# Optimization experiments

Hardware: AMD Instinct MI355X
Metric: run time of the kernel (lower is better)

## Reference

```python
import jax, jax.numpy as jnp
import numpy as np

N = 50000  # nodes == edges (source multiplies [N,H] node tensor by [E] edge attention)
HW = 8


def _adaptive_pool_2x2_from9(h):
    # PyTorch AdaptiveAvgPool2d((2,2)) on 9x9: bins [0:5) and [4:9) per dim (overlap at 4)
    def binpair(t, ax):
        s0 = jnp.take(t, jnp.arange(0, 5), axis=ax).mean(axis=ax)
        s1 = jnp.take(t, jnp.arange(4, 9), axis=ax).mean(axis=ax)
        return jnp.stack([s0, s1], axis=ax)
    return binpair(binpair(h, 3), 2)  # [N,64,2,2]


def _fe_net(x, c1w, c1b, c2w, c2b, fw, fb):
    h = x[:, None, :, :]  # [N,1,8,8]
    h = jax.lax.conv_general_dilated(h, c1w, (1, 1), ((1, 1), (1, 1)),
                                     dimension_numbers=('NCHW', 'OIHW', 'NCHW')) + c1b[None, :, None, None]
    h = jax.nn.relu(h)  # [N,32,8,8]
    h = jax.lax.conv_general_dilated(h, c2w, (1, 1), ((1, 1), (1, 1)),
                                     dimension_numbers=('NCHW', 'OIHW', 'NCHW')) + c2b[None, :, None, None]
    h = jax.nn.relu(h)  # [N,64,9,9]
    h = _adaptive_pool_2x2_from9(h).reshape(h.shape[0], -1)  # [N,256]
    return h @ fw + fb  # [N,32]


def _gcn(x, src, dst, W, b, n):
    h = x @ W
    idx = jnp.arange(n)
    s = jnp.concatenate([src, idx])
    d = jnp.concatenate([dst, idx])
    deg = jax.ops.segment_sum(jnp.ones(s.shape[0], h.dtype), d, num_segments=n)
    dis = jnp.where(deg > 0, jax.lax.rsqrt(jnp.maximum(deg, 1e-12)), 0.0)
    norm = dis[s] * dis[d]
    out = jax.ops.segment_sum(h[s] * norm[:, None], d, num_segments=n)
    return out + b


def _attention1(aux, src, dst, n):
    frame = aux[:, 2]
    fd = jnp.abs(frame[src] - frame[dst])
    outdeg = jax.ops.segment_sum(jnp.ones(src.shape[0], aux.dtype), src, num_segments=n)
    return jnp.where(fd == 1.0, 1.0 / jnp.maximum(outdeg[src], 1.0), 0.0)


def _attention2(aux, src, dst):
    ang, rad, frame = aux[:, 0], aux[:, 1], aux[:, 2]
    fd = jnp.abs(frame[src] - frame[dst])
    dx = rad[dst] * jnp.cos(ang[dst]) - rad[src] * jnp.cos(ang[src])
    dy = rad[dst] * jnp.sin(ang[dst]) - rad[src] * jnp.sin(ang[src])
    fd_safe = jnp.where(fd == 2.0, fd, 1.0)
    vel = jnp.sqrt(dx * dx + dy * dy + 1e-12) / fd_safe
    return jnp.where(fd == 2.0, jnp.exp(-vel / 8.5), 0.0)


def setup_inputs() -> dict:
    key = jax.random.key(0)
    ks = jax.random.split(key, 20)
    x = jax.random.normal(ks[0], (N, HW, HW), jnp.float32)
    angle = jax.random.uniform(ks[1], (N,), jnp.float32, 0.0, 2.0 * np.pi)
    radius = jax.random.uniform(ks[2], (N,), jnp.float32, 1.0, 100.0)
    frame = jax.random.randint(ks[3], (N,), 0, 10).astype(jnp.float32)
    aux_features = jnp.stack([angle, radius, frame], axis=1)
    edge_index = jax.random.randint(ks[4], (2, N), 0, N)
    s = 0.05
    p = lambda k, sh: jax.random.normal(k, sh, jnp.float32) * s
    return {
        'x': x, 'aux_features': aux_features, 'edge_index': edge_index,
        'conv1_w': p(ks[5], (32, 1, 3, 3)), 'conv1_b': jnp.zeros((32,), jnp.float32),
        'conv2_w': p(ks[6], (64, 32, 2, 2)), 'conv2_b': jnp.zeros((64,), jnp.float32),
        'fe_fc_w': p(ks[7], (256, 32)), 'fe_fc_b': jnp.zeros((32,), jnp.float32),
        'gcn1_w': p(ks[8], (32, 64)), 'gcn1_b': jnp.zeros((64,), jnp.float32),
        'gcn2_w': p(ks[9], (64, 64)), 'gcn2_b': jnp.zeros((64,), jnp.float32),
        'fc_w': p(ks[10], (64, 32)), 'fc_b': jnp.zeros((32,), jnp.float32),
        'out_w': p(ks[11], (32, 1)), 'out_b': jnp.zeros((1,), jnp.float32),
    }


def reference(x, aux_features, edge_index, conv1_w, conv1_b, conv2_w, conv2_b,
              fe_fc_w, fe_fc_b, gcn1_w, gcn1_b, gcn2_w, gcn2_b, fc_w, fc_b,
              out_w, out_b):
    n = x.shape[0]
    src, dst = edge_index[0], edge_index[1]
    sig = _fe_net(x, conv1_w, conv1_b, conv2_w, conv2_b, fe_fc_w, fe_fc_b)  # [N,32]
    att1 = _attention1(aux_features, src, dst, n)  # [E] == [N]
    x1 = jax.nn.relu(_gcn(sig, src, dst, gcn1_w, gcn1_b, n) * att1[:, None])
    att2 = _attention2(aux_features, src, dst)
    x2 = jax.nn.relu(_gcn(x1, src, dst, gcn2_w, gcn2_b, n) * att2[:, None])
    h = jax.nn.relu(x2 @ fc_w + fc_b)
    out = jax.nn.sigmoid(h @ out_w + out_b)  # [N,1]
    return out
```

## Files before the change

kernel.cpp:

```cpp
#include <hip/hip_runtime.h>
#include <math.h>

typedef float f32x4 __attribute__((ext_vector_type(4)));
typedef __bf16 bf16x8 __attribute__((ext_vector_type(8)));
typedef unsigned short ushort8 __attribute__((ext_vector_type(8)));
typedef unsigned short ushort4v __attribute__((ext_vector_type(4)));

static __device__ __forceinline__ unsigned short f2bf(float f) {
    unsigned int u = __builtin_bit_cast(unsigned int, f);
    unsigned int lsb = (u >> 16) & 1u;
    u += 0x7fffu + lsb;
    return (unsigned short)(u >> 16);
}

__global__ __launch_bounds__(256, 3) void fe_kernel(
    const float* __restrict__ x,
    const float* __restrict__ w1, const float* __restrict__ b1,
    const float* __restrict__ w2, const float* __restrict__ b2,
    unsigned short* __restrict__ poolbf, int n)
{
    __shared__ float w1t[10][32];
    __shared__ unsigned short hT[4][100][40];
    __shared__ float xs[4][104];

    const int t = threadIdx.x, lane = t & 63, wave = t >> 6;
    const int cl = lane & 15, kg = lane >> 4;

    if (t < 288) w1t[t >> 5][t & 31] = w1[(t & 31) * 9 + (t >> 5)];
    if (t >= 288 && t < 320) w1t[9][t - 288] = b1[t - 288];

    bf16x8 bfr[4][4];
    #pragma unroll
    for (int ct = 0; ct < 4; ++ct)
        #pragma unroll
        for (int tap = 0; tap < 4; ++tap) {
            const float* gp = w2 + (size_t)(ct * 16 + cl) * 128 + kg * 32 + tap;
            ushort8 u;
            #pragma unroll
            for (int e = 0; e < 8; ++e) u[e] = f2bf(gp[e * 4]);
            bfr[ct][tap] = __builtin_bit_cast(bf16x8, u);
        }
    float b2r[4];
    #pragma unroll
    for (int ct = 0; ct < 4; ++ct) b2r[ct] = b2[ct * 16 + cl];

    {
        ushort8 z8 = {0,0,0,0,0,0,0,0};
        for (int r = lane; r < 100; r += 64) {
            const int pi = r / 10, pj = r - 10 * (r / 10);
            if (pi == 0 || pi == 9 || pj == 0 || pj == 9) {
                *reinterpret_cast<ushort8*>(&hT[wave][r][0])  = z8;
                *reinterpret_cast<ushort8*>(&hT[wave][r][8])  = z8;
                *reinterpret_cast<ushort8*>(&hT[wave][r][16]) = z8;
                *reinterpret_cast<ushort8*>(&hT[wave][r][24]) = z8;
                xs[wave][r] = 0.0f;
            }
        }
    }
    __syncthreads();

    const int i = lane >> 3, j = lane & 7;
    const int rr = (i + 1) * 10 + (j + 1);
    const int gw = blockIdx.x * 4 + wave;
    const int nw = gridDim.x * 4;

    for (int node = gw; node < n; node += nw) {
        xs[wave][rr] = x[(size_t)node * 64 + lane];
        asm volatile("s_waitcnt lgkmcnt(0)" ::: "memory");

        float xv[9];
        #pragma unroll
        for (int ki = 0; ki < 3; ++ki)
            #pragma unroll
            for (int kj = 0; kj < 3; ++kj)
                xv[ki * 3 + kj] = xs[wave][(i + ki) * 10 + (j + kj)];

        #pragma unroll
        for (int cp = 0; cp < 4; ++cp) {
            ushort8 hv;
            #pragma unroll
            for (int half = 0; half < 2; ++half) {
                const int cg = cp * 2 + half;
                f32x4 s = *reinterpret_cast<const f32x4*>(&w1t[9][cg * 4]);
                #pragma unroll
                for (int q = 0; q < 9; ++q) {
                    const f32x4 wq = *reinterpret_cast<const f32x4*>(&w1t[q][cg * 4]);
                    s += xv[q] * wq;
                }
                #pragma unroll
                for (int c = 0; c < 4; ++c)
                    hv[half * 4 + c] = f2bf(fmaxf(s[c], 0.0f));
            }
            *reinterpret_cast<ushort8*>(&hT[wave][rr][cp * 8]) = hv;
        }
        asm volatile("s_waitcnt lgkmcnt(0)" ::: "memory");

        float pb[4][4];
        #pragma unroll
        for (int ct = 0; ct < 4; ++ct)
            #pragma unroll
            for (int b = 0; b < 4; ++b) pb[ct][b] = 0.0f;

        #pragma unroll
        for (int mt = 0; mt < 6; ++mt) {
            const int p = mt * 16 + cl;
            const int ia = p / 9, ja = p - ia * 9;
            const int rb = (p < 81) ? (ia * 10 + ja) : 0;

            f32x4 acc[4];
            #pragma unroll
            for (int ct = 0; ct < 4; ++ct)
                acc[ct] = (f32x4){b2r[ct], b2r[ct], b2r[ct], b2r[ct]};

            #pragma unroll
            for (int tap = 0; tap < 4; ++tap) {
                const bf16x8 afr = *reinterpret_cast<const bf16x8*>(
                    &hT[wave][rb + (tap >> 1) * 10 + (tap & 1)][kg * 8]);
                #pragma unroll
                for (int ct = 0; ct < 4; ++ct)
                    acc[ct] = __builtin_amdgcn_mfma_f32_16x16x32_bf16(
                        afr, bfr[ct][tap], acc[ct], 0, 0, 0);
            }

            #pragma unroll
            for (int rg = 0; rg < 4; ++rg) {
                if (mt * 16 + rg >= 81) continue;
                const int pd = mt * 16 + (kg << 2) + rg;
                const int id = pd / 9, jd = pd - id * 9;
                const bool val = pd < 81;
                const float wa = (val && id <= 4 && jd <= 4) ? 1.0f : 0.0f;
                const float wb = (val && id <= 4 && jd >= 4) ? 1.0f : 0.0f;
                const float wc = (val && id >= 4 && jd <= 4) ? 1.0f : 0.0f;
                const float wd = (val && id >= 4 && jd >= 4) ? 1.0f : 0.0f;
                #pragma unroll
                for (int ct = 0; ct < 4; ++ct) {
                    const float v = fmaxf(acc[ct][rg], 0.0f);
                    pb[ct][0] = fmaf(v, wa, pb[ct][0]);
                    pb[ct][1] = fmaf(v, wb, pb[ct][1]);
                    pb[ct][2] = fmaf(v, wc, pb[ct][2]);
                    pb[ct][3] = fmaf(v, wd, pb[ct][3]);
                }
            }
        }

        #pragma unroll
        for (int ct = 0; ct < 4; ++ct)
            #pragma unroll
            for (int b = 0; b < 4; ++b) {
                pb[ct][b] += __shfl_xor(pb[ct][b], 16);
                pb[ct][b] += __shfl_xor(pb[ct][b], 32);
            }
        ushort4v pv;
        #pragma unroll
        for (int b = 0; b < 4; ++b) {
            const float q = (kg == 0) ? pb[0][b] : (kg == 1) ? pb[1][b]
                          : (kg == 2) ? pb[2][b] : pb[3][b];
            pv[b] = f2bf(q);
        }
        *reinterpret_cast<ushort4v*>(poolbf + (size_t)node * 256 + lane * 4) = pv;
    }
}

__global__ void pre_k(const float* __restrict__ fw, const float* __restrict__ fb,
                      const float* __restrict__ g1w, const float* __restrict__ g2w,
                      unsigned short* __restrict__ W1t, float* __restrict__ v1,
                      unsigned short* __restrict__ W2t)
{
    const int b = blockIdx.x, t = threadIdx.x;
    if (b < 64) {
        float s = 0.0f;
        for (int jj = 0; jj < 32; ++jj) s += fw[t * 32 + jj] * g1w[jj * 64 + b];
        W1t[b * 256 + t] = f2bf(0.04f * s);
    } else {
        const int idx = (b - 64) * 256 + t;
        const int nc = idx >> 6, k = idx & 63;
        W2t[nc * 64 + k] = f2bf(g2w[k * 64 + nc]);
        if (b == 64 && t < 64) {
            float s = 0.0f;
            for (int jj = 0; jj < 32; ++jj) s += fb[jj] * g1w[jj * 64 + t];
            v1[t] = s;
        }
    }
}

template<int NKS, bool HASV>
__global__ __launch_bounds__(256) void mm_k(
    const unsigned short* __restrict__ A, const unsigned short* __restrict__ Bt,
    const float* __restrict__ v1, float* __restrict__ h, int n)
{
    const int lane = threadIdx.x & 63;
    const int cl = lane & 15, kg = lane >> 4;
    const int gw = blockIdx.x * 4 + (threadIdx.x >> 6);
    const int nw = gridDim.x * 4;
    const int K = NKS * 32;
    const int ntiles = (n + 15) >> 4;

    float vv[4];
    #pragma unroll
    for (int nt = 0; nt < 4; ++nt) vv[nt] = HASV ? v1[nt * 16 + cl] : 0.0f;

    for (int mt = gw; mt < ntiles; mt += nw) {
        const int r = min(mt * 16 + cl, n - 1);
        const unsigned short* ar = A + (size_t)r * K + kg * 8;
        f32x4 acc[4];
        #pragma unroll
        for (int nt = 0; nt < 4; ++nt)
            acc[nt] = (f32x4){vv[nt], vv[nt], vv[nt], vv[nt]};
        #pragma unroll
        for (int ks = 0; ks < NKS; ++ks) {
            const bf16x8 afr = *reinterpret_cast<const bf16x8*>(ar + ks * 32);
            #pragma unroll
            for (int nt = 0; nt < 4; ++nt) {
                const bf16x8 bfr = *reinterpret_cast<const bf16x8*>(
                    Bt + (size_t)(nt * 16 + cl) * K + ks * 32 + kg * 8);
                acc[nt] = __builtin_amdgcn_mfma_f32_16x16x32_bf16(afr, bfr, acc[nt], 0, 0, 0);
            }
        }
        #pragma unroll
        for (int nt = 0; nt < 4; ++nt)
            #pragma unroll
            for (int rg = 0; rg < 4; ++rg) {
                const int row = mt * 16 + (kg << 2) + rg;
                if (row < n) h[(size_t)row * 64 + nt * 16 + cl] = acc[nt][rg];
            }
    }
}

__global__ void zero_k(float* __restrict__ p, int n)
{
    int idx = blockIdx.x * blockDim.x + threadIdx.x;
    if (idx < n) p[idx] = 0.0f;
}

__global__ void count_k(const int* __restrict__ ei, float* __restrict__ outdeg,
                        float* __restrict__ indeg, int m)
{
    int e = blockIdx.x * blockDim.x + threadIdx.x;
    if (e >= m) return;
    atomicAdd(&outdeg[ei[e]], 1.0f);
    atomicAdd(&indeg[ei[m + e]], 1.0f);
}

__global__ void prep_k(const float* __restrict__ indeg, float* __restrict__ dis, int n)
{
    int idx = blockIdx.x * blockDim.x + threadIdx.x;
    if (idx < n) dis[idx] = rsqrtf(indeg[idx] + 1.0f);
}

__global__ void att_k(const float* __restrict__ aux, const int* __restrict__ ei,
                      const float* __restrict__ outdeg,
                      float* __restrict__ att1, float* __restrict__ att2, int m)
{
    int e = blockIdx.x * blockDim.x + threadIdx.x;
    if (e >= m) return;
    const int s = ei[e], d = ei[m + e];
    const float fs = aux[(size_t)s * 3 + 2], fdd = aux[(size_t)d * 3 + 2];
    const float fd = fabsf(fs - fdd);
    att1[e] = (fd == 1.0f) ? (1.0f / fmaxf(outdeg[s], 1.0f)) : 0.0f;
    const float angs = aux[(size_t)s * 3 + 0], rads = aux[(size_t)s * 3 + 1];
    const float angd = aux[(size_t)d * 3 + 0], radd = aux[(size_t)d * 3 + 1];
    const float dx = radd * cosf(angd) - rads * cosf(angs);
    const float dy = radd * sinf(angd) - rads * sinf(angs);
    const float vel = sqrtf(dx * dx + dy * dy + 1e-12f) * 0.5f;
    att2[e] = (fd == 2.0f) ? expf(-vel / 8.5f) : 0.0f;
}

__global__ void accinit_k(const float* __restrict__ h, const float* __restrict__ dis,
                          const float* __restrict__ b, float* __restrict__ acc, int n)
{
    size_t idx = (size_t)blockIdx.x * blockDim.x + threadIdx.x;
    if (idx >= (size_t)n * 64) return;
    const int node = (int)(idx >> 6), k = (int)(idx & 63);
    const float di = dis[node];
    acc[idx] = b[k] + di * di * h[idx];
}

__global__ void scatter_k(const float* __restrict__ h, const int* __restrict__ ei,
                          const float* __restrict__ dis, float* __restrict__ acc, int m)
{
    size_t idx = (size_t)blockIdx.x * blockDim.x + threadIdx.x;
    if (idx >= (size_t)m * 64) return;
    const int e = (int)(idx >> 6), k = (int)(idx & 63);
    const int s = ei[e], d = ei[m + e];
    const float w = dis[s] * dis[d];
    atomicAdd(&acc[(size_t)d * 64 + k], w * h[(size_t)s * 64 + k]);
}

__global__ void fin_k(float* __restrict__ acc, const float* __restrict__ att,
                      unsigned short* __restrict__ xout, int n)
{
    size_t idx = (size_t)blockIdx.x * blockDim.x + threadIdx.x;
    if (idx >= (size_t)n * 64) return;
    const int node = (int)(idx >> 6);
    const float v = fmaxf(acc[idx] * att[node], 0.0f);
    if (xout) xout[idx] = f2bf(v);
    else      acc[idx] = v;
}

__global__ void head_k(const float* __restrict__ x2, const float* __restrict__ fcw,
                       const float* __restrict__ fcb, const float* __restrict__ outw,
                       const float* __restrict__ outb, float* __restrict__ out, int n)
{
    size_t idx = (size_t)blockIdx.x * blockDim.x + threadIdx.x;
    const int node = (int)(idx >> 5), o = (int)(idx & 31);
    if (node >= n) return;
    const float* xr = x2 + (size_t)node * 64;
    float s = fcb[o];
    #pragma unroll
    for (int k = 0; k < 64; ++k) s = fmaf(xr[k], fcw[k * 32 + o], s);
    s = fmaxf(s, 0.0f);
    float p = s * outw[o];
    #pragma unroll
    for (int mk = 16; mk >= 1; mk >>= 1) p += __shfl_xor(p, mk);
    if (o == 0) out[node] = 1.0f / (1.0f + expf(-(p + outb[0])));
}

extern "C" void kernel_launch(void* const* d_in, const int* in_sizes, int n_in,
                              void* d_out, int out_size, void* d_ws, size_t ws_size,
                              hipStream_t stream)
{
    const float* x    = (const float*)d_in[0];
    const float* aux  = (const float*)d_in[1];
    const int*   ei   = (const int*)  d_in[2];
    const float* c1w  = (const float*)d_in[3];
    const float* c1b  = (const float*)d_in[4];
    const float* c2w  = (const float*)d_in[5];
    const float* c2b  = (const float*)d_in[6];
    const float* few  = (const float*)d_in[7];
    const float* feb  = (const float*)d_in[8];
    const float* g1w  = (const float*)d_in[9];
    const float* g1b  = (const float*)d_in[10];
    const float* g2w  = (const float*)d_in[11];
    const float* g2b  = (const float*)d_in[12];
    const float* fcw  = (const float*)d_in[13];
    const float* fcb  = (const float*)d_in[14];
    const float* outw = (const float*)d_in[15];
    const float* outb = (const float*)d_in[16];
    float* out = (float*)d_out;

    const int n = in_sizes[0] / 64;
    const int m = in_sizes[2] / 2;

    float* ws = (float*)d_ws;
    unsigned short* poolbf = (unsigned short*)ws;
    float* acc  = ws;
    unsigned short* x1bf = (unsigned short*)(ws + (size_t)n * 64);
    float* h    = ws + (size_t)n * 128;
    unsigned short* W1t = (unsigned short*)(ws + (size_t)n * 192);
    float* v1   = ws + (size_t)n * 192 + 8192;
    unsigned short* W2t = (unsigned short*)(v1 + 64);
    float* outdeg = v1 + 64 + 2048;
    float* indeg  = outdeg + n;
    float* dis    = indeg + n;
    float* att1   = dis + n;
    float* att2   = att1 + m;

    const dim3 b256(256);
    const int gE   = (m + 255) / 256;
    const int gNn  = (n + 255) / 256;
    const int gNM  = (int)(((size_t)n * 64 + 255) / 256);
    const int gEM  = (int)(((size_t)m * 64 + 255) / 256);
    const int gNH  = (int)(((size_t)n * 32 + 255) / 256);
    const int gMM  = (((n + 15) / 16) + 3) / 4;

    pre_k<<<80, b256, 0, stream>>>(few, feb, g1w, g2w, W1t, v1, W2t);
    fe_kernel<<<768, b256, 0, stream>>>(x, c1w, c1b, c2w, c2b, poolbf, n);

    zero_k<<<(2 * n + 255) / 256, b256, 0, stream>>>(outdeg, 2 * n);
    count_k<<<gE, b256, 0, stream>>>(ei, outdeg, indeg, m);
    prep_k<<<gNn, b256, 0, stream>>>(indeg, dis, n);
    att_k<<<gE, b256, 0, stream>>>(aux, ei, outdeg, att1, att2, m);

    mm_k<8, true><<<gMM, b256, 0, stream>>>(poolbf, W1t, v1, h, n);
    accinit_k<<<gNM, b256, 0, stream>>>(h, dis, g1b, acc, n);
    scatter_k<<<gEM, b256, 0, stream>>>(h, ei, dis, acc, m);
    fin_k<<<gNM, b256, 0, stream>>>(acc, att1, x1bf, n);

    mm_k<2, false><<<gMM, b256, 0, stream>>>(x1bf, W2t, nullptr, h, n);
    accinit_k<<<gNM, b256, 0, stream>>>(h, dis, g2b, acc, n);
    scatter_k<<<gEM, b256, 0, stream>>>(h, ei, dis, acc, m);
    fin_k<<<gNM, b256, 0, stream>>>(acc, att2, nullptr, n);

    head_k<<<gNH, b256, 0, stream>>>(acc, fcw, fcb, outw, outb, out, n);
}
```

Baseline: 287.0 us.

## Move conv1 to MFMA via im2col, prefetch inputs, and streamline pooling reduction

The first 3x3 convolution now builds a per-wave im2col tile through lane shuffles and runs it as bf16 MFMA instead of scalar FMAs over LDS. The next node's input row is prefetched in a register, and the pooling bin masks and conv2 row bases are computed once and held in registers. The cross-lane pooling reduction now uses a transposed exchange that halves the shuffle count. It also switches to the hardware bf16 convert and zeroes all of LDS without a block barrier. This aims to cut VALU work in fe_kernel, at the cost of conv1 inputs being rounded to bf16 and more register pressure.

```diff
diff --git a/kernel.cpp b/kernel.cpp
--- a/kernel.cpp
+++ b/kernel.cpp
@@ -2,15 +2,13 @@
 #include <math.h>
 
 typedef float f32x4 __attribute__((ext_vector_type(4)));
+typedef float f32x2 __attribute__((ext_vector_type(2)));
 typedef __bf16 bf16x8 __attribute__((ext_vector_type(8)));
 typedef unsigned short ushort8 __attribute__((ext_vector_type(8)));
 typedef unsigned short ushort4v __attribute__((ext_vector_type(4)));
 
-static __device__ __forceinline__ unsigned short f2bf(float f) {
-    unsigned int u = __builtin_bit_cast(unsigned int, f);
-    unsigned int lsb = (u >> 16) & 1u;
-    u += 0x7fffu + lsb;
-    return (unsigned short)(u >> 16);
+static __device__ __forceinline__ unsigned short bfbits(float f) {
+    return __builtin_bit_cast(unsigned short, (__bf16)f);
 }
 
 __global__ __launch_bounds__(256, 3) void fe_kernel(
@@ -19,145 +17,187 @@
     const float* __restrict__ w2, const float* __restrict__ b2,
     unsigned short* __restrict__ poolbf, int n)
 {
-    __shared__ float w1t[10][32];
     __shared__ unsigned short hT[4][100][40];
-    __shared__ float xs[4][104];
+    __shared__ unsigned short xim[4][64][40];
 
     const int t = threadIdx.x, lane = t & 63, wave = t >> 6;
     const int cl = lane & 15, kg = lane >> 4;
-
-    if (t < 288) w1t[t >> 5][t & 31] = w1[(t & 31) * 9 + (t >> 5)];
-    if (t >= 288 && t < 320) w1t[9][t - 288] = b1[t - 288];
-
-    bf16x8 bfr[4][4];
-    #pragma unroll
-    for (int ct = 0; ct < 4; ++ct)
+    const int i = lane >> 3, j = lane & 7;
+
+    for (int e = lane; e < 100 * 40; e += 64) (&hT[wave][0][0])[e] = 0;
+    for (int e = lane; e < 64 * 40; e += 64) (&xim[wave][0][0])[e] = 0;
+
+    bf16x8 w1f[2]; float b1r[2];
+    #pragma unroll
+    for (int ct = 0; ct < 2; ++ct) {
+        ushort8 u;
+        #pragma unroll
+        for (int e = 0; e < 8; ++e) {
+            const int tap = kg * 8 + e;
+            u[e] = (tap < 9) ? bfbits(w1[(ct * 16 + cl) * 9 + tap]) : (unsigned short)0;
+        }
+        w1f[ct] = __builtin_bit_cast(bf16x8, u);
+        b1r[ct] = b1[ct * 16 + cl];
+    }
+
+    bf16x8 bfr[4][4]; float b2r[4];
+    #pragma unroll
+    for (int ct = 0; ct < 4; ++ct) {
         #pragma unroll
         for (int tap = 0; tap < 4; ++tap) {
-            const float* gp = w2 + (size_t)(ct * 16 + cl) * 128 + kg * 32 + tap;
             ushort8 u;
             #pragma unroll
-            for (int e = 0; e < 8; ++e) u[e] = f2bf(gp[e * 4]);
+            for (int e = 0; e < 8; ++e) {
+                const int pos = kg * 8 + e;
+                const int ci = ((pos & 1) << 4) | (pos >> 1);
+                u[e] = bfbits(w2[(size_t)(ct * 16 + cl) * 128 + ci * 4 + tap]);
+            }
             bfr[ct][tap] = __builtin_bit_cast(bf16x8, u);
         }
-    float b2r[4];
-    #pragma unroll
-    for (int ct = 0; ct < 4; ++ct) b2r[ct] = b2[ct * 16 + cl];
-
+        b2r[ct] = b2[ct * 16 + cl];
+    }
+
+    ushort8 vmask; unsigned short m8;
     {
-        ushort8 z8 = {0,0,0,0,0,0,0,0};
-        for (int r = lane; r < 100; r += 64) {
-            const int pi = r / 10, pj = r - 10 * (r / 10);
-            if (pi == 0 || pi == 9 || pj == 0 || pj == 9) {
-                *reinterpret_cast<ushort8*>(&hT[wave][r][0])  = z8;
-                *reinterpret_cast<ushort8*>(&hT[wave][r][8])  = z8;
-                *reinterpret_cast<ushort8*>(&hT[wave][r][16]) = z8;
-                *reinterpret_cast<ushort8*>(&hT[wave][r][24]) = z8;
-                xs[wave][r] = 0.0f;
-            }
-        }
-    }
-    __syncthreads();
-
-    const int i = lane >> 3, j = lane & 7;
-    const int rr = (i + 1) * 10 + (j + 1);
+        #pragma unroll
+        for (int q = 0; q < 9; ++q) {
+            const int ki = q / 3, kj = q - 3 * (q / 3);
+            const int ri = i + ki - 1, cj = j + kj - 1;
+            const unsigned short ok = (ri >= 0 && ri < 8 && cj >= 0 && cj < 8) ? 0xFFFFu : 0;
+            if (q < 8) vmask[q] = ok; else m8 = ok;
+        }
+    }
+
+    unsigned int pm[3] = {0u, 0u, 0u};
+    #pragma unroll
+    for (int mt = 0; mt < 6; ++mt)
+        #pragma unroll
+        for (int rg = 0; rg < 4; ++rg) {
+            const int slot = mt * 4 + rg;
+            const int pd = mt * 16 + kg * 4 + rg;
+            unsigned int bits = 0;
+            if (pd < 81) {
+                const int id = pd / 9, jd = pd - 9 * (pd / 9);
+                if (id <= 4 && jd <= 4) bits |= 1u;
+                if (id <= 4 && jd >= 4) bits |= 2u;
+                if (id >= 4 && jd <= 4) bits |= 4u;
+                if (id >= 4 && jd >= 4) bits |= 8u;
+            }
+            pm[slot >> 3] |= bits << ((slot & 7) * 4);
+        }
+
+    int rbase[6];
+    #pragma unroll
+    for (int mt = 0; mt < 6; ++mt) {
+        const int p = mt * 16 + cl;
+        const int ia = p / 9, ja = p - 9 * ia;
+        rbase[mt] = (p < 81) ? (ia * 10 + ja) : 0;
+    }
+
     const int gw = blockIdx.x * 4 + wave;
     const int nw = gridDim.x * 4;
 
+    float v = (gw < n) ? x[(size_t)gw * 64 + lane] : 0.0f;
+
     for (int node = gw; node < n; node += nw) {
-        xs[wave][rr] = x[(size_t)node * 64 + lane];
+        const int nn = node + nw;
+        const float vnext = x[(size_t)(nn < n ? nn : node) * 64 + lane];
+
+        float tv[9];
+        tv[0] = __shfl(v, lane - 9); tv[1] = __shfl(v, lane - 8); tv[2] = __shfl(v, lane - 7);
+        tv[3] = __shfl(v, lane - 1); tv[4] = v;                   tv[5] = __shfl(v, lane + 1);
+        tv[6] = __shfl(v, lane + 7); tv[7] = __shfl(v, lane + 8); tv[8] = __shfl(v, lane + 9);
+        ushort8 pk;
+        #pragma unroll
+        for (int q = 0; q < 8; ++q) pk[q] = bfbits(tv[q]);
+        pk &= vmask;
+        *reinterpret_cast<ushort8*>(&xim[wave][lane][0]) = pk;
+        xim[wave][lane][8] = bfbits(tv[8]) & m8;
+
         asm volatile("s_waitcnt lgkmcnt(0)" ::: "memory");
 
-        float xv[9];
-        #pragma unroll
-        for (int ki = 0; ki < 3; ++ki)
-            #pragma unroll
-            for (int kj = 0; kj < 3; ++kj)
-                xv[ki * 3 + kj] = xs[wave][(i + ki) * 10 + (j + kj)];
-
-        #pragma unroll
-        for (int cp = 0; cp < 4; ++cp) {
-            ushort8 hv;
-            #pragma unroll
-            for (int half = 0; half < 2; ++half) {
-                const int cg = cp * 2 + half;
-                f32x4 s = *reinterpret_cast<const f32x4*>(&w1t[9][cg * 4]);
-                #pragma unroll
-                for (int q = 0; q < 9; ++q) {
-                    const f32x4 wq = *reinterpret_cast<const f32x4*>(&w1t[q][cg * 4]);
-                    s += xv[q] * wq;
-                }
-                #pragma unroll
-                for (int c = 0; c < 4; ++c)
-                    hv[half * 4 + c] = f2bf(fmaxf(s[c], 0.0f));
-            }
-            *reinterpret_cast<ushort8*>(&hT[wave][rr][cp * 8]) = hv;
+        #pragma unroll
+        for (int mt = 0; mt < 4; ++mt) {
+            const bf16x8 afr = *reinterpret_cast<const bf16x8*>(&xim[wave][mt * 16 + cl][kg * 8]);
+            f32x4 a0 = {b1r[0], b1r[0], b1r[0], b1r[0]};
+            f32x4 a1 = {b1r[1], b1r[1], b1r[1], b1r[1]};
+            a0 = __builtin_amdgcn_mfma_f32_16x16x32_bf16(afr, w1f[0], a0, 0, 0, 0);
+            a1 = __builtin_amdgcn_mfma_f32_16x16x32_bf16(afr, w1f[1], a1, 0, 0, 0);
+            #pragma unroll
+            for (int rg = 0; rg < 4; ++rg) {
+                const int pdx = mt * 16 + kg * 4 + rg;
+                const int row = ((pdx >> 3) + 1) * 10 + (pdx & 7) + 1;
+                const unsigned int packed =
+                    (unsigned int)bfbits(fmaxf(a0[rg], 0.0f)) |
+                    ((unsigned int)bfbits(fmaxf(a1[rg], 0.0f)) << 16);
+                *reinterpret_cast<unsigned int*>(&hT[wave][row][cl * 2]) = packed;
+            }
         }
         asm volatile("s_waitcnt lgkmcnt(0)" ::: "memory");
 
-        float pb[4][4];
-        #pragma unroll
-        for (int ct = 0; ct < 4; ++ct)
-            #pragma unroll
-            for (int b = 0; b < 4; ++b) pb[ct][b] = 0.0f;
+        f32x2 pb01[4], pb23[4];
+        #pragma unroll
+        for (int ct = 0; ct < 4; ++ct) { pb01[ct] = (f32x2){0.f, 0.f}; pb23[ct] = (f32x2){0.f, 0.f}; }
 
         #pragma unroll
         for (int mt = 0; mt < 6; ++mt) {
-            const int p = mt * 16 + cl;
-            const int ia = p / 9, ja = p - ia * 9;
-            const int rb = (p < 81) ? (ia * 10 + ja) : 0;
+            const int rb = rbase[mt];
+            bf16x8 a[4];
+            a[0] = *reinterpret_cast<const bf16x8*>(&hT[wave][rb][kg * 8]);
+            a[1] = *reinterpret_cast<const bf16x8*>(&hT[wave][rb + 1][kg * 8]);
+            a[2] = *reinterpret_cast<const bf16x8*>(&hT[wave][rb + 10][kg * 8]);
+            a[3] = *reinterpret_cast<const bf16x8*>(&hT[wave][rb + 11][kg * 8]);
 
             f32x4 acc[4];
             #pragma unroll
             for (int ct = 0; ct < 4; ++ct)
                 acc[ct] = (f32x4){b2r[ct], b2r[ct], b2r[ct], b2r[ct]};
-
-            #pragma unroll
-            for (int tap = 0; tap < 4; ++tap) {
-                const bf16x8 afr = *reinterpret_cast<const bf16x8*>(
-                    &hT[wave][rb + (tap >> 1) * 10 + (tap & 1)][kg * 8]);
+            #pragma unroll
+            for (int tap = 0; tap < 4; ++tap)
                 #pragma unroll
                 for (int ct = 0; ct < 4; ++ct)
-                    acc[ct] = __builtin_amdgcn_mfma_f32_16x16x32_bf16(
-                        afr, bfr[ct][tap], acc[ct], 0, 0, 0);
-            }
+                    acc[ct] = __builtin_amdgcn_mfma_f32_16x16x32_bf16(a[tap], bfr[ct][tap], acc[ct], 0, 0, 0);
 
             #pragma unroll
             for (int rg = 0; rg < 4; ++rg) {
                 if (mt * 16 + rg >= 81) continue;
-                const int pd = mt * 16 + (kg << 2) + rg;
-                const int id = pd / 9, jd = pd - id * 9;
-                const bool val = pd < 81;
-                const float wa = (val && id <= 4 && jd <= 4) ? 1.0f : 0.0f;
-                const float wb = (val && id <= 4 && jd >= 4) ? 1.0f : 0.0f;
-                const float wc = (val && id >= 4 && jd <= 4) ? 1.0f : 0.0f;
-                const float wd = (val && id >= 4 && jd >= 4) ? 1.0f : 0.0f;
+                const int slot = mt * 4 + rg;
+                const unsigned int bits = pm[slot >> 3] >> ((slot & 7) * 4);
+                const f32x2 w01 = {(float)(bits & 1u), (float)((bits >> 1) & 1u)};
+                const f32x2 w23 = {(float)((bits >> 2) & 1u), (float)((bits >> 3) & 1u)};
                 #pragma unroll
                 for (int ct = 0; ct < 4; ++ct) {
-                    const float v = fmaxf(acc[ct][rg], 0.0f);
-                    pb[ct][0] = fmaf(v, wa, pb[ct][0]);
-                    pb[ct][1] = fmaf(v, wb, pb[ct][1]);
-                    pb[ct][2] = fmaf(v, wc, pb[ct][2]);
-                    pb[ct][3] = fmaf(v, wd, pb[ct][3]);
+                    const float vr = fmaxf(acc[ct][rg], 0.0f);
+                    const f32x2 v2 = {vr, vr};
+                    pb01[ct] += v2 * w01;
+                    pb23[ct] += v2 * w23;
                 }
             }
         }
 
-        #pragma unroll
-        for (int ct = 0; ct < 4; ++ct)
-            #pragma unroll
-            for (int b = 0; b < 4; ++b) {
-                pb[ct][b] += __shfl_xor(pb[ct][b], 16);
-                pb[ct][b] += __shfl_xor(pb[ct][b], 32);
-            }
+        const bool k0 = (kg & 1) != 0;
+        const bool k1 = (kg & 2) != 0;
+        float outb[4];
+        #pragma unroll
+        for (int b = 0; b < 4; ++b) {
+            const float x0 = (b < 2) ? pb01[0][b] : pb23[0][b - 2];
+            const float x1 = (b < 2) ? pb01[1][b] : pb23[1][b - 2];
+            const float x2 = (b < 2) ? pb01[2][b] : pb23[2][b - 2];
+            const float x3 = (b < 2) ? pb01[3][b] : pb23[3][b - 2];
+            float keepA = k0 ? x1 : x0, sendA = k0 ? x0 : x1;
+            float keepB = k0 ? x3 : x2, sendB = k0 ? x2 : x3;
+            keepA += __shfl_xor(sendA, 16);
+            keepB += __shfl_xor(sendB, 16);
+            float keep = k1 ? keepB : keepA, send = k1 ? keepA : keepB;
+            keep += __shfl_xor(send, 32);
+            outb[b] = keep;
+        }
         ushort4v pv;
         #pragma unroll
-        for (int b = 0; b < 4; ++b) {
-            const float q = (kg == 0) ? pb[0][b] : (kg == 1) ? pb[1][b]
-                          : (kg == 2) ? pb[2][b] : pb[3][b];
-            pv[b] = f2bf(q);
-        }
+        for (int b = 0; b < 4; ++b) pv[b] = bfbits(outb[b]);
         *reinterpret_cast<ushort4v*>(poolbf + (size_t)node * 256 + lane * 4) = pv;
+
+        v = vnext;
     }
 }
 
@@ -170,11 +210,11 @@
     if (b < 64) {
         float s = 0.0f;
         for (int jj = 0; jj < 32; ++jj) s += fw[t * 32 + jj] * g1w[jj * 64 + b];
-        W1t[b * 256 + t] = f2bf(0.04f * s);
+        W1t[b * 256 + t] = bfbits(0.04f * s);
     } else {
         const int idx = (b - 64) * 256 + t;
         const int nc = idx >> 6, k = idx & 63;
-        W2t[nc * 64 + k] = f2bf(g2w[k * 64 + nc]);
+        W2t[nc * 64 + k] = bfbits(g2w[k * 64 + nc]);
         if (b == 64 && t < 64) {
             float s = 0.0f;
             for (int jj = 0; jj < 32; ++jj) s += fb[jj] * g1w[jj * 64 + t];
@@ -211,9 +251,9 @@
             const bf16x8 afr = *reinterpret_cast<const bf16x8*>(ar + ks * 32);
             #pragma unroll
             for (int nt = 0; nt < 4; ++nt) {
-                const bf16x8 bfr = *reinterpret_cast<const bf16x8*>(
+                const bf16x8 bfrg = *reinterpret_cast<const bf16x8*>(
                     Bt + (size_t)(nt * 16 + cl) * K + ks * 32 + kg * 8);
-                acc[nt] = __builtin_amdgcn_mfma_f32_16x16x32_bf16(afr, bfr, acc[nt], 0, 0, 0);
+                acc[nt] = __builtin_amdgcn_mfma_f32_16x16x32_bf16(afr, bfrg, acc[nt], 0, 0, 0);
             }
         }
         #pragma unroll
@@ -293,7 +333,7 @@
     if (idx >= (size_t)n * 64) return;
     const int node = (int)(idx >> 6);
     const float v = fmaxf(acc[idx] * att[node], 0.0f);
-    if (xout) xout[idx] = f2bf(v);
+    if (xout) xout[idx] = bfbits(v);
     else      acc[idx] = v;
 }
 
```

Result: slower. 329.0 us (+14.6%).
